# Kernel optimization log

Hardware: AMD Instinct MI355X
Metric: run time of the kernel (lower is better)

## Reference

```python
import jax, jax.numpy as jnp
import numpy as np

B, N, NH = 16, 2048, 64
DROP = 0.1


def setup_inputs() -> dict:
    key = jax.random.key(0)
    ks = jax.random.split(key, 10)
    s = 1.0 / np.sqrt(NH)
    return {
        "adj": jax.random.normal(ks[0], (B, N, N), jnp.float32) * 0.02,
        "diff": jax.random.normal(ks[1], (B, N, N), jnp.float32) * 0.02,
        "sub_local_pos1": jax.random.normal(ks[2], (B, N, NH), jnp.float32),
        "sub_local_pos2": jax.random.normal(ks[3], (B, N, NH), jnp.float32),
        "sub_local_neg1": jax.random.normal(ks[4], (B, N, NH), jnp.float32),
        "sub_local_neg2": jax.random.normal(ks[5], (B, N, NH), jnp.float32),
        # Bilinear params: weight [1, NH, NH], bias [1] (xavier-ish scale)
        "W0": jax.random.normal(ks[6], (1, NH, NH), jnp.float32) * s,
        "b0": jnp.zeros((1,), jnp.float32),
        "W1": jax.random.normal(ks[7], (1, NH, NH), jnp.float32) * s,
        "b1": jnp.zeros((1,), jnp.float32),
        "W2": jax.random.normal(ks[8], (1, NH, NH), jnp.float32) * s,
        "b2": jnp.zeros((1,), jnp.float32),
        "alpha": jnp.full((1,), 0.5, jnp.float32),
        "beta": jnp.full((1,), 0.5, jnp.float32),
        "lamda": jnp.full((1,), 0.5, jnp.float32),
        "k": 0.5,  # static fraction kept per topk cascade
    }


def _bilinear(x, y, W, b):
    # nn.Bilinear(NH, NH, 1): out[b,n] = x[b,n,:] @ W[0] @ y[b,n,:] + b[0]
    return jnp.einsum('bni,ij,bnj->bn', x, W[0], y) + b[0]


def _select(X, idx):
    # Select module: sort indices along batch dim 0, then per-row gather
    idx = jnp.sort(idx, axis=0)
    return jnp.take_along_axis(X, idx[:, :, None], axis=1)


def _topk_idx(logits, k_frac):
    half = logits.shape[1] // 2
    score = jax.nn.sigmoid(logits[:, half:] - logits[:, :half])  # neg - pos
    _, idx_pos = jax.lax.top_k(score, half)
    return idx_pos[:, : int(k_frac * half)]


def _forward(adj, diff, pos1, pos2, neg1, neg2,
             W0, b0, W1, b1, W2, b2, alpha, beta, lamda, k):
    mkey = jax.random.key(1)
    m1 = jax.random.uniform(jax.random.fold_in(mkey, 0), (N, NH)) < DROP
    m2 = jax.random.uniform(jax.random.fold_in(mkey, 1), (N, NH)) < DROP
    p1 = jnp.where(m1, 0.0, pos1); n1 = jnp.where(m1, 0.0, neg1)
    p2 = jnp.where(m2, 0.0, pos2); n2 = jnp.where(m2, 0.0, neg2)

    fus_pos = (p1 + p2) * 0.5
    fus_neg = (n1 + n2) * 0.5

    # Readout = mean over node dim, then sigmoid, broadcast back to [B,N,NH]
    g1 = jnp.broadcast_to(jax.nn.sigmoid(jnp.mean(p1, axis=1))[:, None, :], p1.shape)
    g2 = jnp.broadcast_to(jax.nn.sigmoid(jnp.mean(p2, axis=1))[:, None, :], p2.shape)

    lf1 = jnp.concatenate([_bilinear(fus_pos, g1, W0, b0), _bilinear(fus_neg, g1, W0, b0)], 1)
    lf2 = jnp.concatenate([_bilinear(fus_pos, g2, W0, b0), _bilinear(fus_neg, g2, W0, b0)], 1)
    logits_fusion = alpha * lf1 + (1.0 - alpha) * lf2  # [B, 2N]

    idx = _topk_idx(logits_fusion, k)  # [B, K1]

    sel_pos = _select(fus_pos, idx)
    sel_neg = _select(fus_neg, idx)
    l1 = _select(jax.nn.sigmoid(jnp.einsum('bnm,bmh->bnh', adj, p1)), idx)
    l2 = _select(jax.nn.sigmoid(jnp.einsum('bnm,bmh->bnh', diff, p2)), idx)

    ls1 = jnp.concatenate([_bilinear(sel_pos, l1, W1, b1), _bilinear(sel_neg, l1, W1, b1)], 1)
    ls2 = jnp.concatenate([_bilinear(sel_pos, l2, W1, b1), _bilinear(sel_neg, l2, W1, b1)], 1)
    logits_fusion_sub = beta * ls1 + (1.0 - beta) * ls2  # [B, 2*K1]

    idx_sub = _topk_idx(logits_fusion_sub, k)  # [B, K2]

    sel_pos_sub = _select(sel_pos, idx_sub)
    sel_neg_sub = _select(sel_neg, idx_sub)
    l1s = _select(_select(jax.nn.sigmoid(p1), idx), idx_sub)
    l2s = _select(_select(jax.nn.sigmoid(p2), idx), idx_sub)

    lss1 = jnp.concatenate([_bilinear(sel_pos_sub, l1s, W2, b2), _bilinear(sel_neg_sub, l1s, W2, b2)], 1)
    lss2 = jnp.concatenate([_bilinear(sel_pos_sub, l2s, W2, b2), _bilinear(sel_neg_sub, l2s, W2, b2)], 1)
    logits_fusion_sub_sub = lamda * lss1 + (1.0 - lamda) * lss2  # [B, 2*K2]

    return (logits_fusion, logits_fusion_sub, logits_fusion_sub_sub)


def reference(adj, diff, sub_local_pos1, sub_local_pos2, sub_local_neg1, sub_local_neg2,
              W0, b0, W1, b1, W2, b2, alpha, beta, lamda, k):
    return _forward(adj, diff, sub_local_pos1, sub_local_pos2, sub_local_neg1, sub_local_neg2,
                    W0, b0, W1, b1, W2, b2, alpha, beta, lamda, k)
```

## Files before the change

### kernel.cpp

```cpp
#include <hip/hip_runtime.h>
#include <cstdint>
#include <cstddef>

static constexpr int Bn  = 16;
static constexpr int Nn  = 2048;
static constexpr int NHn = 64;
static constexpr int K1  = 1024;
static constexpr int K2  = 512;

__host__ __device__ inline void tf2x32(uint32_t k0, uint32_t k1, uint32_t& x0, uint32_t& x1) {
  const uint32_t ks0 = k0, ks1 = k1, ks2 = k0 ^ k1 ^ 0x1BD11BDAu;
  x0 += ks0; x1 += ks1;
  const int R[20] = {13,15,26,6, 17,29,16,24, 13,15,26,6, 17,29,16,24, 13,15,26,6};
  const uint32_t ks[3] = {ks0, ks1, ks2};
  int inj = 0;
  for (int r = 0; r < 20; ++r) {
    x0 += x1;
    x1 = (x1 << R[r]) | (x1 >> (32 - R[r]));
    x1 ^= x0;
    if ((r & 3) == 3) {
      ++inj;
      x0 += ks[inj % 3];
      x1 += ks[(inj + 1) % 3] + (uint32_t)inj;
    }
  }
}

__device__ __forceinline__ float xla_expf(float x) {
  const float LOG2EF   = 1.44269504088896341f;
  const float ln2_hi   = 0.693359375f;
  const float nln2_lo  = 2.12194440e-4f;
  const float p0 = 1.9875691500e-4f, p1c = 1.3981999507e-3f, p2c = 8.3334519073e-3f,
              p3c = 4.1665795894e-2f, p4c = 1.6666665459e-1f, p5c = 5.0000001201e-1f;
  float xc = fminf(fmaxf(x, -87.33654785f), 88.72283935f);
  float m = floorf(__fmaf_rn(xc, LOG2EF, 0.5f));
  float r = __fmaf_rn(m, -ln2_hi, xc);
  r = __fmaf_rn(m, nln2_lo, r);
  float r2 = __fmul_rn(r, r);
  float y = p0;
  y = __fmaf_rn(y, r, p1c);
  y = __fmaf_rn(y, r, p2c);
  y = __fmaf_rn(y, r, p3c);
  y = __fmaf_rn(y, r, p4c);
  y = __fmaf_rn(y, r, p5c);
  y = __fmaf_rn(y, r2, r);
  y = __fadd_rn(y, 1.0f);
  int n = (int)m;
  float s2 = __uint_as_float((uint32_t)(n + 127) << 23);
  return __fmul_rn(y, s2);
}

__device__ __forceinline__ float sigmoid_exp(float x) {
  float e = xla_expf(-x);
  return __fdiv_rn(1.0f, __fadd_rn(1.0f, e));
}

__device__ __forceinline__ unsigned long long pack_key(float s, int idx) {
  return ((unsigned long long)(__float_as_uint(s) ^ 0xFFFFFFFFu) << 32) | (uint32_t)idx;
}

__global__ void mask_kernel(uint32_t fk0a, uint32_t fk1a, uint32_t fk0b, uint32_t fk1b,
                            float* __restrict__ mask1, float* __restrict__ mask2) {
  int i = blockIdx.x * blockDim.x + threadIdx.x;
  if (i >= Nn * NHn) return;
  uint32_t x0 = 0u, x1 = (uint32_t)i;
  tf2x32(fk0a, fk1a, x0, x1);
  uint32_t bits = x0 ^ x1;
  float u = __uint_as_float((bits >> 9) | 0x3f800000u) - 1.0f;
  mask1[i] = (u < 0.1f) ? 1.0f : 0.0f;
  x0 = 0u; x1 = (uint32_t)i;
  tf2x32(fk0b, fk1b, x0, x1);
  bits = x0 ^ x1;
  u = __uint_as_float((bits >> 9) | 0x3f800000u) - 1.0f;
  mask2[i] = (u < 0.1f) ? 1.0f : 0.0f;
}

__global__ void drop_kernel(const float* __restrict__ pos1, const float* __restrict__ pos2,
                            const float* __restrict__ mask1, const float* __restrict__ mask2,
                            float* __restrict__ p1, float* __restrict__ p2) {
  size_t i = (size_t)blockIdx.x * blockDim.x + threadIdx.x;
  int nh = (int)(i & (size_t)(Nn * NHn - 1));
  p1[i] = (mask1[nh] != 0.0f) ? 0.0f : pos1[i];
  p2[i] = (mask2[nh] != 0.0f) ? 0.0f : pos2[i];
}

__global__ void gmean_kernel(const float* __restrict__ p1, const float* __restrict__ p2,
                             float* __restrict__ g1, float* __restrict__ g2) {
  int b = blockIdx.x, h = threadIdx.x;
  const float* P1 = p1 + (size_t)b * Nn * NHn + h;
  const float* P2 = p2 + (size_t)b * Nn * NHn + h;
  float a1 = 0.0f, a2 = 0.0f;
  for (int n = 0; n < Nn; n += 8) {
    float v1[8], v2[8];
#pragma unroll
    for (int u = 0; u < 8; ++u) {
      v1[u] = P1[(size_t)(n + u) * NHn];
      v2[u] = P2[(size_t)(n + u) * NHn];
    }
#pragma unroll
    for (int u = 0; u < 8; ++u) {
      a1 = __fadd_rn(a1, v1[u]);
      a2 = __fadd_rn(a2, v2[u]);
    }
  }
  float m1 = __fdiv_rn(a1, 2048.0f);
  float m2 = __fdiv_rn(a2, 2048.0f);
  g1[b * 64 + h] = sigmoid_exp(m1);
  g2[b * 64 + h] = sigmoid_exp(m2);
}

__global__ __launch_bounds__(256) void logits1_np(
    const float* __restrict__ p1, const float* __restrict__ p2,
    const float* __restrict__ neg1, const float* __restrict__ neg2,
    const float* __restrict__ mask1, const float* __restrict__ mask2,
    const float* __restrict__ g1, const float* __restrict__ g2,
    const float* __restrict__ W0, const float* __restrict__ b0p,
    const float* __restrict__ alphap,
    float* __restrict__ out0, unsigned long long* __restrict__ key1) {
  __shared__ __align__(16) float xp[64][68], xn[64][68], w[4096], g[2][64];
  int b = blockIdx.y, n0 = blockIdx.x * 64, t = threadIdx.x;
  for (int c = 0; c < 16; ++c) {
    int idx = c * 256 + t, row = idx >> 6, i = idx & 63;
    size_t ga = ((size_t)b * Nn + n0 + row) * NHn + i;
    int ma = (n0 + row) * NHn + i;
    xp[row][i] = __fmul_rn(__fadd_rn(p1[ga], p2[ga]), 0.5f);
    float nv1 = (mask1[ma] != 0.0f) ? 0.0f : neg1[ga];
    float nv2 = (mask2[ma] != 0.0f) ? 0.0f : neg2[ga];
    xn[row][i] = __fmul_rn(__fadd_rn(nv1, nv2), 0.5f);
    w[idx] = W0[idx];
  }
  if (t < 64) { g[0][t] = g1[b * 64 + t]; g[1][t] = g2[b * 64 + t]; }
  __syncthreads();
  int row = t >> 2, e = t & 3;
  const float* x = (e & 2) ? &xn[row][0] : &xp[row][0];
  const float* gg = g[e & 1];
  float T[64];
#pragma unroll
  for (int j = 0; j < 64; ++j) T[j] = 0.0f;
  for (int i = 0; i < 64; ++i) {
    float xv = x[i];
#pragma unroll
    for (int jb = 0; jb < 16; ++jb) {
      float4 wv = *(const float4*)&w[i * 64 + jb * 4];
      T[jb * 4 + 0] = __fmaf_rn(xv, wv.x, T[jb * 4 + 0]);
      T[jb * 4 + 1] = __fmaf_rn(xv, wv.y, T[jb * 4 + 1]);
      T[jb * 4 + 2] = __fmaf_rn(xv, wv.z, T[jb * 4 + 2]);
      T[jb * 4 + 3] = __fmaf_rn(xv, wv.w, T[jb * 4 + 3]);
    }
  }
  float acc = 0.0f;
#pragma unroll
  for (int jb = 0; jb < 16; ++jb) {
    float4 gv = *(const float4*)&gg[jb * 4];
    acc = __fadd_rn(acc, __fmul_rn(T[jb * 4 + 0], gv.x));
    acc = __fadd_rn(acc, __fmul_rn(T[jb * 4 + 1], gv.y));
    acc = __fadd_rn(acc, __fmul_rn(T[jb * 4 + 2], gv.z));
    acc = __fadd_rn(acc, __fmul_rn(T[jb * 4 + 3], gv.w));
  }
  float a = __fadd_rn(acc, *b0p);
  float al = *alphap, om = __fsub_rn(1.0f, al);
  float other = __shfl_xor(a, 1);
  float L = __fadd_rn(__fmul_rn(al, a), __fmul_rn(om, other));
  float Lneg = __shfl_xor(L, 2);
  int n = n0 + row;
  if (e == 0) {
    out0[(size_t)b * (2 * Nn) + n] = L;
    float d = __fsub_rn(Lneg, L);
    key1[(size_t)b * Nn + n] = pack_key(sigmoid_exp(d), n);
  } else if (e == 2) {
    out0[(size_t)b * (2 * Nn) + Nn + n] = L;
  }
}

template <int S>
__global__ void topk_bitonic(const unsigned long long* __restrict__ keysrc,
                             int* __restrict__ idx_out) {
  constexpr int K = S / 2;
  __shared__ unsigned long long keys[S];
  int b = blockIdx.x;
  for (int i = threadIdx.x; i < S; i += blockDim.x)
    keys[i] = keysrc[(size_t)b * S + i];
  for (int k = 2; k <= S; k <<= 1) {
    for (int j = k >> 1; j > 0; j >>= 1) {
      __syncthreads();
      for (int t = threadIdx.x; t < S / 2; t += blockDim.x) {
        int i = ((t / j) * (j << 1)) + (t % j);
        unsigned long long a = keys[i], c = keys[i + j];
        if (((i & k) == 0) == (a > c)) { keys[i] = c; keys[i + j] = a; }
      }
    }
  }
  __syncthreads();
  for (int t = threadIdx.x; t < K; t += blockDim.x)
    idx_out[(size_t)b * K + t] = (int)(keys[t] & 0xffffffffu);
}

__global__ void colsort_kernel(const int* __restrict__ idx, int* __restrict__ sidx, int K) {
  int j = blockIdx.x * blockDim.x + threadIdx.x;
  if (j >= K) return;
  int v[16];
  for (int b = 0; b < 16; ++b) v[b] = idx[b * K + j];
  for (int a = 1; a < 16; ++a) {
    int x = v[a]; int c = a - 1;
    while (c >= 0 && v[c] > x) { v[c + 1] = v[c]; --c; }
    v[c + 1] = x;
  }
  for (int b = 0; b < 16; ++b) sidx[b * K + j] = v[b];
}

__global__ __launch_bounds__(256) void selmm_np3(const float* __restrict__ M,
                                                 const float* __restrict__ P,
                                                 const int* __restrict__ sidx,
                                                 float* __restrict__ L) {
  __shared__ __align__(16) float ash[32][132];
  __shared__ __align__(16) float psh[128][64];
  __shared__ int rj[32];
  int b = blockIdx.y, j0 = blockIdx.x * 32, t = threadIdx.x;
  if (t < 32) rj[t] = sidx[b * K1 + j0 + t];
  __syncthreads();
  int cg = t & 15, rg = t >> 4;
  int r0 = rg * 2, r1 = r0 + 1;
  const float* Mb = M + (size_t)b * Nn * Nn;
  const float* Pb = P + (size_t)b * Nn * NHn;
  float acc00 = 0.f, acc01 = 0.f, acc02 = 0.f, acc03 = 0.f;
  float acc10 = 0.f, acc11 = 0.f, acc12 = 0.f, acc13 = 0.f;
  for (int m0 = 0; m0 < Nn; m0 += 128) {
#pragma unroll
    for (int pass = 0; pass < 16; ++pass) {
      int idx = pass * 256 + t;
      int row = idx >> 7, col = idx & 127;
      ash[row][col] = Mb[(size_t)rj[row] * Nn + m0 + col];
    }
#pragma unroll 8
    for (int pass = 0; pass < 32; ++pass) {
      int idx = pass * 256 + t;
      int mm = idx >> 6, hh = idx & 63;
      psh[mm][hh] = Pb[(size_t)(m0 + mm) * NHn + hh];
    }
    __syncthreads();
#pragma unroll 4
    for (int mb = 0; mb < 32; ++mb) {
      float4 a0 = *(const float4*)&ash[r0][mb * 4];
      float4 a1 = *(const float4*)&ash[r1][mb * 4];
      float4 pv0 = *(const float4*)&psh[mb * 4 + 0][cg * 4];
      float4 pv1 = *(const float4*)&psh[mb * 4 + 1][cg * 4];
      float4 pv2 = *(const float4*)&psh[mb * 4 + 2][cg * 4];
      float4 pv3 = *(const float4*)&psh[mb * 4 + 3][cg * 4];
      acc00 = __fmaf_rn(a0.x, pv0.x, acc00);
      acc01 = __fmaf_rn(a0.x, pv0.y, acc01);
      acc02 = __fmaf_rn(a0.x, pv0.z, acc02);
      acc03 = __fmaf_rn(a0.x, pv0.w, acc03);
      acc10 = __fmaf_rn(a1.x, pv0.x, acc10);
      acc11 = __fmaf_rn(a1.x, pv0.y, acc11);
      acc12 = __fmaf_rn(a1.x, pv0.z, acc12);
      acc13 = __fmaf_rn(a1.x, pv0.w, acc13);
      acc00 = __fmaf_rn(a0.y, pv1.x, acc00);
      acc01 = __fmaf_rn(a0.y, pv1.y, acc01);
      acc02 = __fmaf_rn(a0.y, pv1.z, acc02);
      acc03 = __fmaf_rn(a0.y, pv1.w, acc03);
      acc10 = __fmaf_rn(a1.y, pv1.x, acc10);
      acc11 = __fmaf_rn(a1.y, pv1.y, acc11);
      acc12 = __fmaf_rn(a1.y, pv1.z, acc12);
      acc13 = __fmaf_rn(a1.y, pv1.w, acc13);
      acc00 = __fmaf_rn(a0.z, pv2.x, acc00);
      acc01 = __fmaf_rn(a0.z, pv2.y, acc01);
      acc02 = __fmaf_rn(a0.z, pv2.z, acc02);
      acc03 = __fmaf_rn(a0.z, pv2.w, acc03);
      acc10 = __fmaf_rn(a1.z, pv2.x, acc10);
      acc11 = __fmaf_rn(a1.z, pv2.y, acc11);
      acc12 = __fmaf_rn(a1.z, pv2.z, acc12);
      acc13 = __fmaf_rn(a1.z, pv2.w, acc13);
      acc00 = __fmaf_rn(a0.w, pv3.x, acc00);
      acc01 = __fmaf_rn(a0.w, pv3.y, acc01);
      acc02 = __fmaf_rn(a0.w, pv3.z, acc02);
      acc03 = __fmaf_rn(a0.w, pv3.w, acc03);
      acc10 = __fmaf_rn(a1.w, pv3.x, acc10);
      acc11 = __fmaf_rn(a1.w, pv3.y, acc11);
      acc12 = __fmaf_rn(a1.w, pv3.z, acc12);
      acc13 = __fmaf_rn(a1.w, pv3.w, acc13);
    }
    __syncthreads();
  }
  size_t base0 = ((size_t)b * K1 + j0 + r0) * NHn + cg * 4;
  size_t base1 = ((size_t)b * K1 + j0 + r1) * NHn + cg * 4;
  L[base0 + 0] = sigmoid_exp(acc00);
  L[base0 + 1] = sigmoid_exp(acc01);
  L[base0 + 2] = sigmoid_exp(acc02);
  L[base0 + 3] = sigmoid_exp(acc03);
  L[base1 + 0] = sigmoid_exp(acc10);
  L[base1 + 1] = sigmoid_exp(acc11);
  L[base1 + 2] = sigmoid_exp(acc12);
  L[base1 + 3] = sigmoid_exp(acc13);
}

__global__ __launch_bounds__(256) void logits2_np(
    const float* __restrict__ p1, const float* __restrict__ p2,
    const float* __restrict__ neg1, const float* __restrict__ neg2,
    const float* __restrict__ mask1, const float* __restrict__ mask2,
    const int* __restrict__ sidx1,
    const float* __restrict__ l1, const float* __restrict__ l2,
    const float* __restrict__ W1, const float* __restrict__ b1p,
    const float* __restrict__ betap,
    float* __restrict__ out1, unsigned long long* __restrict__ key2) {
  __shared__ __align__(16) float xp[64][68], xn[64][68], y1s[64][68], y2s[64][68], w[4096];
  __shared__ int rrs[64];
  int b = blockIdx.y, j0 = blockIdx.x * 64, t = threadIdx.x;
  if (t < 64) rrs[t] = sidx1[b * K1 + j0 + t];
  __syncthreads();
  for (int c = 0; c < 16; ++c) {
    int idx = c * 256 + t, row = idx >> 6, i = idx & 63;
    int rr = rrs[row];
    size_t ga = ((size_t)b * Nn + rr) * NHn + i;
    int ma = rr * NHn + i;
    xp[row][i] = __fmul_rn(__fadd_rn(p1[ga], p2[ga]), 0.5f);
    float nv1 = (mask1[ma] != 0.0f) ? 0.0f : neg1[ga];
    float nv2 = (mask2[ma] != 0.0f) ? 0.0f : neg2[ga];
    xn[row][i] = __fmul_rn(__fadd_rn(nv1, nv2), 0.5f);
    size_t la = ((size_t)b * K1 + j0 + row) * NHn + i;
    y1s[row][i] = l1[la];
    y2s[row][i] = l2[la];
    w[idx] = W1[idx];
  }
  __syncthreads();
  int row = t >> 2, e = t & 3;
  const float* x = (e & 2) ? &xn[row][0] : &xp[row][0];
  const float* yy = (e & 1) ? &y2s[row][0] : &y1s[row][0];
  float T[64];
#pragma unroll
  for (int j = 0; j < 64; ++j) T[j] = 0.0f;
  for (int i = 0; i < 64; ++i) {
    float xv = x[i];
#pragma unroll
    for (int jb = 0; jb < 16; ++jb) {
      float4 wv = *(const float4*)&w[i * 64 + jb * 4];
      T[jb * 4 + 0] = __fmaf_rn(xv, wv.x, T[jb * 4 + 0]);
      T[jb * 4 + 1] = __fmaf_rn(xv, wv.y, T[jb * 4 + 1]);
      T[jb * 4 + 2] = __fmaf_rn(xv, wv.z, T[jb * 4 + 2]);
      T[jb * 4 + 3] = __fmaf_rn(xv, wv.w, T[jb * 4 + 3]);
    }
  }
  float acc = 0.0f;
#pragma unroll
  for (int jb = 0; jb < 16; ++jb) {
    float4 yv = *(const float4*)&yy[jb * 4];
    acc = __fadd_rn(acc, __fmul_rn(T[jb * 4 + 0], yv.x));
    acc = __fadd_rn(acc, __fmul_rn(T[jb * 4 + 1], yv.y));
    acc = __fadd_rn(acc, __fmul_rn(T[jb * 4 + 2], yv.z));
    acc = __fadd_rn(acc, __fmul_rn(T[jb * 4 + 3], yv.w));
  }
  float a = __fadd_rn(acc, *b1p);
  float be = *betap, om = __fsub_rn(1.0f, be);
  float other = __shfl_xor(a, 1);
  float L = __fadd_rn(__fmul_rn(be, a), __fmul_rn(om, other));
  float Lneg = __shfl_xor(L, 2);
  int j = j0 + row;
  if (e == 0) {
    out1[(size_t)b * (2 * K1) + j] = L;
    float d = __fsub_rn(Lneg, L);
    key2[(size_t)b * K1 + j] = pack_key(sigmoid_exp(d), j);
  } else if (e == 2) {
    out1[(size_t)b * (2 * K1) + K1 + j] = L;
  }
}

__global__ void logits3_kernel(const float* __restrict__ p1, const float* __restrict__ p2,
                               const float* __restrict__ neg1, const float* __restrict__ neg2,
                               const float* __restrict__ mask1, const float* __restrict__ mask2,
                               const int* __restrict__ sidx1, const int* __restrict__ sidx2,
                               const float* __restrict__ W2,
                               const float* __restrict__ b2p, const float* __restrict__ lamp,
                               float* __restrict__ out2) {
  int b = blockIdx.y, tt = blockIdx.x, h = threadIdx.x;
  int rr = sidx1[b * K1 + sidx2[b * K2 + tt]];
  __shared__ float XP[64], XN[64];
  size_t xb = ((size_t)b * Nn + rr) * NHn + h;
  int ma = rr * NHn + h;
  float pv1 = p1[xb], pv2 = p2[xb];
  float nv1 = (mask1[ma] != 0.0f) ? 0.0f : neg1[xb];
  float nv2 = (mask2[ma] != 0.0f) ? 0.0f : neg2[xb];
  XP[h] = (pv1 + pv2) * 0.5f;
  XN[h] = (nv1 + nv2) * 0.5f;
  __syncthreads();
  float tp = 0.f, tn = 0.f;
#pragma unroll 8
  for (int i = 0; i < 64; ++i) {
    float ww = W2[i * 64 + h];
    tp = fmaf(XP[i], ww, tp);
    tn = fmaf(XN[i], ww, tn);
  }
  float y1 = sigmoid_exp(pv1);
  float y2 = sigmoid_exp(pv2);
  float p11 = tp * y1, p12 = tp * y2, p21 = tn * y1, p22 = tn * y2;
  for (int o = 32; o > 0; o >>= 1) {
    p11 += __shfl_down(p11, o);
    p12 += __shfl_down(p12, o);
    p21 += __shfl_down(p21, o);
    p22 += __shfl_down(p22, o);
  }
  if (h == 0) {
    float bb = *b2p, lm = *lamp;
    out2[(size_t)b * (2 * K2) + tt]      = lm * (p11 + bb) + (1.0f - lm) * (p12 + bb);
    out2[(size_t)b * (2 * K2) + K2 + tt] = lm * (p21 + bb) + (1.0f - lm) * (p22 + bb);
  }
}

extern "C" void kernel_launch(void* const* d_in, const int* in_sizes, int n_in,
                              void* d_out, int out_size, void* d_ws, size_t ws_size,
                              hipStream_t stream) {
  (void)in_sizes; (void)n_in; (void)out_size; (void)ws_size;

  const float* adj   = (const float*)d_in[0];
  const float* diff  = (const float*)d_in[1];
  const float* pos1  = (const float*)d_in[2];
  const float* pos2  = (const float*)d_in[3];
  const float* neg1  = (const float*)d_in[4];
  const float* neg2  = (const float*)d_in[5];
  const float* W0    = (const float*)d_in[6];
  const float* b0    = (const float*)d_in[7];
  const float* W1    = (const float*)d_in[8];
  const float* b1    = (const float*)d_in[9];
  const float* W2    = (const float*)d_in[10];
  const float* b2    = (const float*)d_in[11];
  const float* alpha = (const float*)d_in[12];
  const float* beta  = (const float*)d_in[13];
  const float* lamda = (const float*)d_in[14];

  float* out0 = (float*)d_out;
  float* out1 = out0 + Bn * 2 * Nn;
  float* out2 = out1 + Bn * 2 * K1;

  char* w = (char*)d_ws;
  size_t off = 0;
  auto alloc = [&](size_t bytes) -> void* {
    void* p = w + off;
    off += (bytes + 255) & ~(size_t)255;
    return p;
  };
  float* mask1 = (float*)alloc((size_t)Nn * NHn * 4);
  float* mask2 = (float*)alloc((size_t)Nn * NHn * 4);
  float* p1    = (float*)alloc((size_t)Bn * Nn * NHn * 4);
  float* p2    = (float*)alloc((size_t)Bn * Nn * NHn * 4);
  float* g1    = (float*)alloc((size_t)Bn * 64 * 4);
  float* g2    = (float*)alloc((size_t)Bn * 64 * 4);
  unsigned long long* key1 = (unsigned long long*)alloc((size_t)Bn * Nn * 8);
  unsigned long long* key2 = (unsigned long long*)alloc((size_t)Bn * K1 * 8);
  int*   idx1  = (int*)alloc((size_t)Bn * K1 * 4);
  int*   sidx1 = (int*)alloc((size_t)Bn * K1 * 4);
  int*   idx2  = (int*)alloc((size_t)Bn * K2 * 4);
  int*   sidx2 = (int*)alloc((size_t)Bn * K2 * 4);
  float* l1    = (float*)alloc((size_t)Bn * K1 * NHn * 4);
  float* l2    = (float*)alloc((size_t)Bn * K1 * NHn * 4);

  uint32_t fk0a = 0u, fk1a = 0u;
  { uint32_t x0 = 0u, x1 = 0u; tf2x32(0u, 1u, x0, x1); fk0a = x0; fk1a = x1; }
  uint32_t fk0b = 0u, fk1b = 0u;
  { uint32_t x0 = 0u, x1 = 1u; tf2x32(0u, 1u, x0, x1); fk0b = x0; fk1b = x1; }

  mask_kernel<<<(Nn * NHn + 255) / 256, 256, 0, stream>>>(fk0a, fk1a, fk0b, fk1b, mask1, mask2);

  drop_kernel<<<(Bn * Nn * NHn) / 256, 256, 0, stream>>>(pos1, pos2, mask1, mask2, p1, p2);

  gmean_kernel<<<Bn, 64, 0, stream>>>(p1, p2, g1, g2);

  logits1_np<<<dim3(Nn / 64, Bn), 256, 0, stream>>>(p1, p2, neg1, neg2, mask1, mask2,
                                                    g1, g2, W0, b0, alpha, out0, key1);

  topk_bitonic<2048><<<Bn, 1024, 0, stream>>>(key1, idx1);
  colsort_kernel<<<K1 / 256, 256, 0, stream>>>(idx1, sidx1, K1);

  selmm_np3<<<dim3(K1 / 32, Bn), 256, 0, stream>>>(adj, p1, sidx1, l1);
  selmm_np3<<<dim3(K1 / 32, Bn), 256, 0, stream>>>(diff, p2, sidx1, l2);

  logits2_np<<<dim3(K1 / 64, Bn), 256, 0, stream>>>(p1, p2, neg1, neg2, mask1, mask2,
                                                    sidx1, l1, l2, W1, b1, beta, out1, key2);

  topk_bitonic<1024><<<Bn, 512, 0, stream>>>(key2, idx2);
  colsort_kernel<<<K2 / 256, 256, 0, stream>>>(idx2, sidx2, K2);

  logits3_kernel<<<dim3(K2, Bn), 64, 0, stream>>>(p1, p2, neg1, neg2, mask1, mask2,
                                                  sidx1, sidx2, W2, b2, lamda, out2);
}
```

Before: 366.3 us.

## Vectorize loads, enlarge selmm tiles, and rework bilinear logits thread mapping

drop_kernel now moves data as float4, and gmean stages rows through shared memory with coalesced float4 loads instead of strided per-column reads. selmm now computes 64 rows per block with a 4x4 register tile and float4 global-to-shared copies, halving block count and increasing reuse of each P tile. logits1 and logits2 use 128 rows per block, and each thread computes both bilinear terms from one shared T vector. W and g/l vectors are read directly from global/L1 instead of being staged in shared memory. The changes add register pressure and move more traffic onto cache reads of W.

Measured after the change: 398.1 us. +8.7%, slower.

```diff
diff --git a/kernel.cpp b/kernel.cpp
--- a/kernel.cpp
+++ b/kernel.cpp
@@ -75,41 +75,58 @@
   mask2[i] = (u < 0.1f) ? 1.0f : 0.0f;
 }
 
-__global__ void drop_kernel(const float* __restrict__ pos1, const float* __restrict__ pos2,
-                            const float* __restrict__ mask1, const float* __restrict__ mask2,
-                            float* __restrict__ p1, float* __restrict__ p2) {
-  size_t i = (size_t)blockIdx.x * blockDim.x + threadIdx.x;
-  int nh = (int)(i & (size_t)(Nn * NHn - 1));
-  p1[i] = (mask1[nh] != 0.0f) ? 0.0f : pos1[i];
-  p2[i] = (mask2[nh] != 0.0f) ? 0.0f : pos2[i];
-}
-
-__global__ void gmean_kernel(const float* __restrict__ p1, const float* __restrict__ p2,
-                             float* __restrict__ g1, float* __restrict__ g2) {
-  int b = blockIdx.x, h = threadIdx.x;
-  const float* P1 = p1 + (size_t)b * Nn * NHn + h;
-  const float* P2 = p2 + (size_t)b * Nn * NHn + h;
+__global__ void drop_kernel(const float4* __restrict__ pos1, const float4* __restrict__ pos2,
+                            const float4* __restrict__ mask1, const float4* __restrict__ mask2,
+                            float4* __restrict__ p1, float4* __restrict__ p2) {
+  size_t i4 = (size_t)blockIdx.x * blockDim.x + threadIdx.x;
+  int nh4 = (int)(i4 & (size_t)(Nn * NHn / 4 - 1));
+  float4 m1 = mask1[nh4], m2 = mask2[nh4];
+  float4 a = pos1[i4], c = pos2[i4];
+  float4 o1, o2;
+  o1.x = (m1.x != 0.0f) ? 0.0f : a.x;  o1.y = (m1.y != 0.0f) ? 0.0f : a.y;
+  o1.z = (m1.z != 0.0f) ? 0.0f : a.z;  o1.w = (m1.w != 0.0f) ? 0.0f : a.w;
+  o2.x = (m2.x != 0.0f) ? 0.0f : c.x;  o2.y = (m2.y != 0.0f) ? 0.0f : c.y;
+  o2.z = (m2.z != 0.0f) ? 0.0f : c.z;  o2.w = (m2.w != 0.0f) ? 0.0f : c.w;
+  p1[i4] = o1;
+  p2[i4] = o2;
+}
+
+__global__ __launch_bounds__(256) void gmean_kernel(const float* __restrict__ p1,
+                                                    const float* __restrict__ p2,
+                                                    float* __restrict__ g1,
+                                                    float* __restrict__ g2) {
+  __shared__ __align__(16) float s1[32][64], s2[32][64];
+  int b = blockIdx.x, t = threadIdx.x;
+  const float* P1 = p1 + (size_t)b * Nn * NHn;
+  const float* P2 = p2 + (size_t)b * Nn * NHn;
   float a1 = 0.0f, a2 = 0.0f;
-  for (int n = 0; n < Nn; n += 8) {
-    float v1[8], v2[8];
-#pragma unroll
-    for (int u = 0; u < 8; ++u) {
-      v1[u] = P1[(size_t)(n + u) * NHn];
-      v2[u] = P2[(size_t)(n + u) * NHn];
-    }
-#pragma unroll
-    for (int u = 0; u < 8; ++u) {
-      a1 = __fadd_rn(a1, v1[u]);
-      a2 = __fadd_rn(a2, v2[u]);
-    }
-  }
-  float m1 = __fdiv_rn(a1, 2048.0f);
-  float m2 = __fdiv_rn(a2, 2048.0f);
-  g1[b * 64 + h] = sigmoid_exp(m1);
-  g2[b * 64 + h] = sigmoid_exp(m2);
-}
-
-__global__ __launch_bounds__(256) void logits1_np(
+  for (int c = 0; c < Nn / 32; ++c) {
+    __syncthreads();
+#pragma unroll
+    for (int ppp = 0; ppp < 2; ++ppp) {
+      int f = ppp * 256 + t;
+      int row = f >> 4, c4 = f & 15;
+      *(float4*)&s1[row][c4 * 4] = *(const float4*)&P1[(size_t)(c * 32 + row) * NHn + c4 * 4];
+      *(float4*)&s2[row][c4 * 4] = *(const float4*)&P2[(size_t)(c * 32 + row) * NHn + c4 * 4];
+    }
+    __syncthreads();
+    if (t < 64) {
+#pragma unroll
+      for (int u = 0; u < 32; ++u) {
+        a1 = __fadd_rn(a1, s1[u][t]);
+        a2 = __fadd_rn(a2, s2[u][t]);
+      }
+    }
+  }
+  if (t < 64) {
+    float m1 = __fdiv_rn(a1, 2048.0f);
+    float m2 = __fdiv_rn(a2, 2048.0f);
+    g1[b * 64 + t] = sigmoid_exp(m1);
+    g2[b * 64 + t] = sigmoid_exp(m2);
+  }
+}
+
+__global__ __launch_bounds__(256, 2) void logits1_np(
     const float* __restrict__ p1, const float* __restrict__ p2,
     const float* __restrict__ neg1, const float* __restrict__ neg2,
     const float* __restrict__ mask1, const float* __restrict__ mask2,
@@ -117,9 +134,9 @@
     const float* __restrict__ W0, const float* __restrict__ b0p,
     const float* __restrict__ alphap,
     float* __restrict__ out0, unsigned long long* __restrict__ key1) {
-  __shared__ __align__(16) float xp[64][68], xn[64][68], w[4096], g[2][64];
-  int b = blockIdx.y, n0 = blockIdx.x * 64, t = threadIdx.x;
-  for (int c = 0; c < 16; ++c) {
+  __shared__ __align__(16) float xp[128][68], xn[128][68];
+  int b = blockIdx.y, n0 = blockIdx.x * 128, t = threadIdx.x;
+  for (int c = 0; c < 32; ++c) {
     int idx = c * 256 + t, row = idx >> 6, i = idx & 63;
     size_t ga = ((size_t)b * Nn + n0 + row) * NHn + i;
     int ma = (n0 + row) * NHn + i;
@@ -127,13 +144,10 @@
     float nv1 = (mask1[ma] != 0.0f) ? 0.0f : neg1[ga];
     float nv2 = (mask2[ma] != 0.0f) ? 0.0f : neg2[ga];
     xn[row][i] = __fmul_rn(__fadd_rn(nv1, nv2), 0.5f);
-    w[idx] = W0[idx];
-  }
-  if (t < 64) { g[0][t] = g1[b * 64 + t]; g[1][t] = g2[b * 64 + t]; }
-  __syncthreads();
-  int row = t >> 2, e = t & 3;
-  const float* x = (e & 2) ? &xn[row][0] : &xp[row][0];
-  const float* gg = g[e & 1];
+  }
+  __syncthreads();
+  int row = t >> 1, e = t & 1;
+  const float* x = e ? &xn[row][0] : &xp[row][0];
   float T[64];
 #pragma unroll
   for (int j = 0; j < 64; ++j) T[j] = 0.0f;
@@ -141,33 +155,39 @@
     float xv = x[i];
 #pragma unroll
     for (int jb = 0; jb < 16; ++jb) {
-      float4 wv = *(const float4*)&w[i * 64 + jb * 4];
+      float4 wv = *(const float4*)&W0[i * 64 + jb * 4];
       T[jb * 4 + 0] = __fmaf_rn(xv, wv.x, T[jb * 4 + 0]);
       T[jb * 4 + 1] = __fmaf_rn(xv, wv.y, T[jb * 4 + 1]);
       T[jb * 4 + 2] = __fmaf_rn(xv, wv.z, T[jb * 4 + 2]);
       T[jb * 4 + 3] = __fmaf_rn(xv, wv.w, T[jb * 4 + 3]);
     }
   }
-  float acc = 0.0f;
+  const float* G1 = g1 + b * 64;
+  const float* G2 = g2 + b * 64;
+  float acc1 = 0.0f, acc2 = 0.0f;
 #pragma unroll
   for (int jb = 0; jb < 16; ++jb) {
-    float4 gv = *(const float4*)&gg[jb * 4];
-    acc = __fadd_rn(acc, __fmul_rn(T[jb * 4 + 0], gv.x));
-    acc = __fadd_rn(acc, __fmul_rn(T[jb * 4 + 1], gv.y));
-    acc = __fadd_rn(acc, __fmul_rn(T[jb * 4 + 2], gv.z));
-    acc = __fadd_rn(acc, __fmul_rn(T[jb * 4 + 3], gv.w));
-  }
-  float a = __fadd_rn(acc, *b0p);
-  float al = *alphap, om = __fsub_rn(1.0f, al);
-  float other = __shfl_xor(a, 1);
-  float L = __fadd_rn(__fmul_rn(al, a), __fmul_rn(om, other));
-  float Lneg = __shfl_xor(L, 2);
+    float4 gv1 = *(const float4*)&G1[jb * 4];
+    float4 gv2 = *(const float4*)&G2[jb * 4];
+    acc1 = __fadd_rn(acc1, __fmul_rn(T[jb * 4 + 0], gv1.x));
+    acc1 = __fadd_rn(acc1, __fmul_rn(T[jb * 4 + 1], gv1.y));
+    acc1 = __fadd_rn(acc1, __fmul_rn(T[jb * 4 + 2], gv1.z));
+    acc1 = __fadd_rn(acc1, __fmul_rn(T[jb * 4 + 3], gv1.w));
+    acc2 = __fadd_rn(acc2, __fmul_rn(T[jb * 4 + 0], gv2.x));
+    acc2 = __fadd_rn(acc2, __fmul_rn(T[jb * 4 + 1], gv2.y));
+    acc2 = __fadd_rn(acc2, __fmul_rn(T[jb * 4 + 2], gv2.z));
+    acc2 = __fadd_rn(acc2, __fmul_rn(T[jb * 4 + 3], gv2.w));
+  }
+  float b0 = *b0p, al = *alphap, om = __fsub_rn(1.0f, al);
+  float L = __fadd_rn(__fmul_rn(al, __fadd_rn(acc1, b0)),
+                      __fmul_rn(om, __fadd_rn(acc2, b0)));
+  float Lother = __shfl_xor(L, 1);
   int n = n0 + row;
   if (e == 0) {
     out0[(size_t)b * (2 * Nn) + n] = L;
-    float d = __fsub_rn(Lneg, L);
+    float d = __fsub_rn(Lother, L);
     key1[(size_t)b * Nn + n] = pack_key(sigmoid_exp(d), n);
-  } else if (e == 2) {
+  } else {
     out0[(size_t)b * (2 * Nn) + Nn + n] = L;
   }
 }
@@ -208,92 +228,85 @@
   for (int b = 0; b < 16; ++b) sidx[b * K + j] = v[b];
 }
 
-__global__ __launch_bounds__(256) void selmm_np3(const float* __restrict__ M,
+__global__ __launch_bounds__(256) void selmm_np4(const float* __restrict__ M,
                                                  const float* __restrict__ P,
                                                  const int* __restrict__ sidx,
                                                  float* __restrict__ L) {
-  __shared__ __align__(16) float ash[32][132];
+  __shared__ __align__(16) float ash[64][132];
   __shared__ __align__(16) float psh[128][64];
-  __shared__ int rj[32];
-  int b = blockIdx.y, j0 = blockIdx.x * 32, t = threadIdx.x;
-  if (t < 32) rj[t] = sidx[b * K1 + j0 + t];
+  __shared__ int rj[64];
+  int b = blockIdx.y, j0 = blockIdx.x * 64, t = threadIdx.x;
+  if (t < 64) rj[t] = sidx[b * K1 + j0 + t];
   __syncthreads();
   int cg = t & 15, rg = t >> 4;
-  int r0 = rg * 2, r1 = r0 + 1;
   const float* Mb = M + (size_t)b * Nn * Nn;
   const float* Pb = P + (size_t)b * Nn * NHn;
-  float acc00 = 0.f, acc01 = 0.f, acc02 = 0.f, acc03 = 0.f;
-  float acc10 = 0.f, acc11 = 0.f, acc12 = 0.f, acc13 = 0.f;
+  float acc[4][4];
+#pragma unroll
+  for (int r = 0; r < 4; ++r)
+#pragma unroll
+    for (int c = 0; c < 4; ++c) acc[r][c] = 0.0f;
+
   for (int m0 = 0; m0 < Nn; m0 += 128) {
 #pragma unroll
-    for (int pass = 0; pass < 16; ++pass) {
-      int idx = pass * 256 + t;
-      int row = idx >> 7, col = idx & 127;
-      ash[row][col] = Mb[(size_t)rj[row] * Nn + m0 + col];
-    }
-#pragma unroll 8
-    for (int pass = 0; pass < 32; ++pass) {
-      int idx = pass * 256 + t;
-      int mm = idx >> 6, hh = idx & 63;
-      psh[mm][hh] = Pb[(size_t)(m0 + mm) * NHn + hh];
+    for (int pass = 0; pass < 8; ++pass) {
+      int f = pass * 256 + t;
+      int row = f >> 5, c4 = f & 31;
+      *(float4*)&ash[row][c4 * 4] = *(const float4*)&Mb[(size_t)rj[row] * Nn + m0 + c4 * 4];
+    }
+#pragma unroll
+    for (int pass = 0; pass < 8; ++pass) {
+      int f = pass * 256 + t;
+      int mm = f >> 4, c4 = f & 15;
+      *(float4*)&psh[mm][c4 * 4] = *(const float4*)&Pb[(size_t)(m0 + mm) * NHn + c4 * 4];
     }
     __syncthreads();
 #pragma unroll 4
     for (int mb = 0; mb < 32; ++mb) {
-      float4 a0 = *(const float4*)&ash[r0][mb * 4];
-      float4 a1 = *(const float4*)&ash[r1][mb * 4];
+      float4 a0 = *(const float4*)&ash[rg * 4 + 0][mb * 4];
+      float4 a1 = *(const float4*)&ash[rg * 4 + 1][mb * 4];
+      float4 a2 = *(const float4*)&ash[rg * 4 + 2][mb * 4];
+      float4 a3 = *(const float4*)&ash[rg * 4 + 3][mb * 4];
       float4 pv0 = *(const float4*)&psh[mb * 4 + 0][cg * 4];
       float4 pv1 = *(const float4*)&psh[mb * 4 + 1][cg * 4];
       float4 pv2 = *(const float4*)&psh[mb * 4 + 2][cg * 4];
       float4 pv3 = *(const float4*)&psh[mb * 4 + 3][cg * 4];
-      acc00 = __fmaf_rn(a0.x, pv0.x, acc00);
-      acc01 = __fmaf_rn(a0.x, pv0.y, acc01);
-      acc02 = __fmaf_rn(a0.x, pv0.z, acc02);
-      acc03 = __fmaf_rn(a0.x, pv0.w, acc03);
-      acc10 = __fmaf_rn(a1.x, pv0.x, acc10);
-      acc11 = __fmaf_rn(a1.x, pv0.y, acc11);
-      acc12 = __fmaf_rn(a1.x, pv0.z, acc12);
-      acc13 = __fmaf_rn(a1.x, pv0.w, acc13);
-      acc00 = __fmaf_rn(a0.y, pv1.x, acc00);
-      acc01 = __fmaf_rn(a0.y, pv1.y, acc01);
-      acc02 = __fmaf_rn(a0.y, pv1.z, acc02);
-      acc03 = __fmaf_rn(a0.y, pv1.w, acc03);
-      acc10 = __fmaf_rn(a1.y, pv1.x, acc10);
-      acc11 = __fmaf_rn(a1.y, pv1.y, acc11);
-      acc12 = __fmaf_rn(a1.y, pv1.z, acc12);
-      acc13 = __fmaf_rn(a1.y, pv1.w, acc13);
-      acc00 = __fmaf_rn(a0.z, pv2.x, acc00);
-      acc01 = __fmaf_rn(a0.z, pv2.y, acc01);
-      acc02 = __fmaf_rn(a0.z, pv2.z, acc02);
-      acc03 = __fmaf_rn(a0.z, pv2.w, acc03);
-      acc10 = __fmaf_rn(a1.z, pv2.x, acc10);
-      acc11 = __fmaf_rn(a1.z, pv2.y, acc11);
-      acc12 = __fmaf_rn(a1.z, pv2.z, acc12);
-      acc13 = __fmaf_rn(a1.z, pv2.w, acc13);
-      acc00 = __fmaf_rn(a0.w, pv3.x, acc00);
-      acc01 = __fmaf_rn(a0.w, pv3.y, acc01);
-      acc02 = __fmaf_rn(a0.w, pv3.z, acc02);
-      acc03 = __fmaf_rn(a0.w, pv3.w, acc03);
-      acc10 = __fmaf_rn(a1.w, pv3.x, acc10);
-      acc11 = __fmaf_rn(a1.w, pv3.y, acc11);
-      acc12 = __fmaf_rn(a1.w, pv3.z, acc12);
-      acc13 = __fmaf_rn(a1.w, pv3.w, acc13);
+#define STEP(q, aq, pq)                                        \
+      acc[0][0] = __fmaf_rn(a0.aq, pq.x, acc[0][0]);           \
+      acc[0][1] = __fmaf_rn(a0.aq, pq.y, acc[0][1]);           \
+      acc[0][2] = __fmaf_rn(a0.aq, pq.z, acc[0][2]);           \
+      acc[0][3] = __fmaf_rn(a0.aq, pq.w, acc[0][3]);           \
+      acc[1][0] = __fmaf_rn(a1.aq, pq.x, acc[1][0]);           \
+      acc[1][1] = __fmaf_rn(a1.aq, pq.y, acc[1][1]);           \
+      acc[1][2] = __fmaf_rn(a1.aq, pq.z, acc[1][2]);           \
+      acc[1][3] = __fmaf_rn(a1.aq, pq.w, acc[1][3]);           \
+      acc[2][0] = __fmaf_rn(a2.aq, pq.x, acc[2][0]);           \
+      acc[2][1] = __fmaf_rn(a2.aq, pq.y, acc[2][1]);           \
+      acc[2][2] = __fmaf_rn(a2.aq, pq.z, acc[2][2]);           \
+      acc[2][3] = __fmaf_rn(a2.aq, pq.w, acc[2][3]);           \
+      acc[3][0] = __fmaf_rn(a3.aq, pq.x, acc[3][0]);           \
+      acc[3][1] = __fmaf_rn(a3.aq, pq.y, acc[3][1]);           \
+      acc[3][2] = __fmaf_rn(a3.aq, pq.z, acc[3][2]);           \
+      acc[3][3] = __fmaf_rn(a3.aq, pq.w, acc[3][3]);
+      STEP(0, x, pv0)
+      STEP(1, y, pv1)
+      STEP(2, z, pv2)
+      STEP(3, w, pv3)
+#undef STEP
     }
     __syncthreads();
   }
-  size_t base0 = ((size_t)b * K1 + j0 + r0) * NHn + cg * 4;
-  size_t base1 = ((size_t)b * K1 + j0 + r1) * NHn + cg * 4;
-  L[base0 + 0] = sigmoid_exp(acc00);
-  L[base0 + 1] = sigmoid_exp(acc01);
-  L[base0 + 2] = sigmoid_exp(acc02);
-  L[base0 + 3] = sigmoid_exp(acc03);
-  L[base1 + 0] = sigmoid_exp(acc10);
-  L[base1 + 1] = sigmoid_exp(acc11);
-  L[base1 + 2] = sigmoid_exp(acc12);
-  L[base1 + 3] = sigmoid_exp(acc13);
-}
-
-__global__ __launch_bounds__(256) void logits2_np(
+#pragma unroll
+  for (int r = 0; r < 4; ++r) {
+    size_t base = ((size_t)b * K1 + j0 + rg * 4 + r) * NHn + cg * 4;
+    L[base + 0] = sigmoid_exp(acc[r][0]);
+    L[base + 1] = sigmoid_exp(acc[r][1]);
+    L[base + 2] = sigmoid_exp(acc[r][2]);
+    L[base + 3] = sigmoid_exp(acc[r][3]);
+  }
+}
+
+__global__ __launch_bounds__(256, 2) void logits2_np(
     const float* __restrict__ p1, const float* __restrict__ p2,
     const float* __restrict__ neg1, const float* __restrict__ neg2,
     const float* __restrict__ mask1, const float* __restrict__ mask2,
@@ -302,12 +315,12 @@
     const float* __restrict__ W1, const float* __restrict__ b1p,
     const float* __restrict__ betap,
     float* __restrict__ out1, unsigned long long* __restrict__ key2) {
-  __shared__ __align__(16) float xp[64][68], xn[64][68], y1s[64][68], y2s[64][68], w[4096];
-  __shared__ int rrs[64];
-  int b = blockIdx.y, j0 = blockIdx.x * 64, t = threadIdx.x;
-  if (t < 64) rrs[t] = sidx1[b * K1 + j0 + t];
-  __syncthreads();
-  for (int c = 0; c < 16; ++c) {
+  __shared__ __align__(16) float xp[128][68], xn[128][68];
+  __shared__ int rrs[128];
+  int b = blockIdx.y, j0 = blockIdx.x * 128, t = threadIdx.x;
+  if (t < 128) rrs[t] = sidx1[b * K1 + j0 + t];
+  __syncthreads();
+  for (int c = 0; c < 32; ++c) {
     int idx = c * 256 + t, row = idx >> 6, i = idx & 63;
     int rr = rrs[row];
     size_t ga = ((size_t)b * Nn + rr) * NHn + i;
@@ -316,15 +329,10 @@
     float nv1 = (mask1[ma] != 0.0f) ? 0.0f : neg1[ga];
     float nv2 = (mask2[ma] != 0.0f) ? 0.0f : neg2[ga];
     xn[row][i] = __fmul_rn(__fadd_rn(nv1, nv2), 0.5f);
-    size_t la = ((size_t)b * K1 + j0 + row) * NHn + i;
-    y1s[row][i] = l1[la];
-    y2s[row][i] = l2[la];
-    w[idx] = W1[idx];
-  }
-  __syncthreads();
-  int row = t >> 2, e = t & 3;
-  const float* x = (e & 2) ? &xn[row][0] : &xp[row][0];
-  const float* yy = (e & 1) ? &y2s[row][0] : &y1s[row][0];
+  }
+  __syncthreads();
+  int row = t >> 1, e = t & 1;
+  const float* x = e ? &xn[row][0] : &xp[row][0];
   float T[64];
 #pragma unroll
   for (int j = 0; j < 64; ++j) T[j] = 0.0f;
@@ -332,33 +340,39 @@
     float xv = x[i];
 #pragma unroll
     for (int jb = 0; jb < 16; ++jb) {
-      float4 wv = *(const float4*)&w[i * 64 + jb * 4];
+      float4 wv = *(const float4*)&W1[i * 64 + jb * 4];
       T[jb * 4 + 0] = __fmaf_rn(xv, wv.x, T[jb * 4 + 0]);
       T[jb * 4 + 1] = __fmaf_rn(xv, wv.y, T[jb * 4 + 1]);
       T[jb * 4 + 2] = __fmaf_rn(xv, wv.z, T[jb * 4 + 2]);
       T[jb * 4 + 3] = __fmaf_rn(xv, wv.w, T[jb * 4 + 3]);
     }
   }
-  float acc = 0.0f;
+  const float* Y1 = l1 + ((size_t)b * K1 + j0 + row) * NHn;
+  const float* Y2 = l2 + ((size_t)b * K1 + j0 + row) * NHn;
+  float acc1 = 0.0f, acc2 = 0.0f;
 #pragma unroll
   for (int jb = 0; jb < 16; ++jb) {
-    float4 yv = *(const float4*)&yy[jb * 4];
-    acc = __fadd_rn(acc, __fmul_rn(T[jb * 4 + 0], yv.x));
-    acc = __fadd_rn(acc, __fmul_rn(T[jb * 4 + 1], yv.y));
-    acc = __fadd_rn(acc, __fmul_rn(T[jb * 4 + 2], yv.z));
-    acc = __fadd_rn(acc, __fmul_rn(T[jb * 4 + 3], yv.w));
-  }
-  float a = __fadd_rn(acc, *b1p);
-  float be = *betap, om = __fsub_rn(1.0f, be);
-  float other = __shfl_xor(a, 1);
-  float L = __fadd_rn(__fmul_rn(be, a), __fmul_rn(om, other));
-  float Lneg = __shfl_xor(L, 2);
+    float4 yv1 = *(const float4*)&Y1[jb * 4];
+    float4 yv2 = *(const float4*)&Y2[jb * 4];
+    acc1 = __fadd_rn(acc1, __fmul_rn(T[jb * 4 + 0], yv1.x));
+    acc1 = __fadd_rn(acc1, __fmul_rn(T[jb * 4 + 1], yv1.y));
+    acc1 = __fadd_rn(acc1, __fmul_rn(T[jb * 4 + 2], yv1.z));
+    acc1 = __fadd_rn(acc1, __fmul_rn(T[jb * 4 + 3], yv1.w));
+    acc2 = __fadd_rn(acc2, __fmul_rn(T[jb * 4 + 0], yv2.x));
+    acc2 = __fadd_rn(acc2, __fmul_rn(T[jb * 4 + 1], yv2.y));
+    acc2 = __fadd_rn(acc2, __fmul_rn(T[jb * 4 + 2], yv2.z));
+    acc2 = __fadd_rn(acc2, __fmul_rn(T[jb * 4 + 3], yv2.w));
+  }
+  float bb = *b1p, be = *betap, om = __fsub_rn(1.0f, be);
+  float L = __fadd_rn(__fmul_rn(be, __fadd_rn(acc1, bb)),
+                      __fmul_rn(om, __fadd_rn(acc2, bb)));
+  float Lother = __shfl_xor(L, 1);
   int j = j0 + row;
   if (e == 0) {
     out1[(size_t)b * (2 * K1) + j] = L;
-    float d = __fsub_rn(Lneg, L);
+    float d = __fsub_rn(Lother, L);
     key2[(size_t)b * K1 + j] = pack_key(sigmoid_exp(d), j);
-  } else if (e == 2) {
+  } else {
     out1[(size_t)b * (2 * K1) + K1 + j] = L;
   }
 }
@@ -458,21 +472,23 @@
 
   mask_kernel<<<(Nn * NHn + 255) / 256, 256, 0, stream>>>(fk0a, fk1a, fk0b, fk1b, mask1, mask2);
 
-  drop_kernel<<<(Bn * Nn * NHn) / 256, 256, 0, stream>>>(pos1, pos2, mask1, mask2, p1, p2);
-
-  gmean_kernel<<<Bn, 64, 0, stream>>>(p1, p2, g1, g2);
-
-  logits1_np<<<dim3(Nn / 64, Bn), 256, 0, stream>>>(p1, p2, neg1, neg2, mask1, mask2,
-                                                    g1, g2, W0, b0, alpha, out0, key1);
+  drop_kernel<<<(Bn * Nn * NHn / 4) / 256, 256, 0, stream>>>(
+      (const float4*)pos1, (const float4*)pos2, (const float4*)mask1, (const float4*)mask2,
+      (float4*)p1, (float4*)p2);
+
+  gmean_kernel<<<Bn, 256, 0, stream>>>(p1, p2, g1, g2);
+
+  logits1_np<<<dim3(Nn / 128, Bn), 256, 0, stream>>>(p1, p2, neg1, neg2, mask1, mask2,
+                                                     g1, g2, W0, b0, alpha, out0, key1);
 
   topk_bitonic<2048><<<Bn, 1024, 0, stream>>>(key1, idx1);
   colsort_kernel<<<K1 / 256, 256, 0, stream>>>(idx1, sidx1, K1);
 
-  selmm_np3<<<dim3(K1 / 32, Bn), 256, 0, stream>>>(adj, p1, sidx1, l1);
-  selmm_np3<<<dim3(K1 / 32, Bn), 256, 0, stream>>>(diff, p2, sidx1, l2);
-
-  logits2_np<<<dim3(K1 / 64, Bn), 256, 0, stream>>>(p1, p2, neg1, neg2, mask1, mask2,
-                                                    sidx1, l1, l2, W1, b1, beta, out1, key2);
+  selmm_np4<<<dim3(K1 / 64, Bn), 256, 0, stream>>>(adj, p1, sidx1, l1);
+  selmm_np4<<<dim3(K1 / 64, Bn), 256, 0, stream>>>(diff, p2, sidx1, l2);
+
+  logits2_np<<<dim3(K1 / 128, Bn), 256, 0, stream>>>(p1, p2, neg1, neg2, mask1, mask2,
+                                                     sidx1, l1, l2, W1, b1, beta, out1, key2);
 
   topk_bitonic<1024><<<Bn, 512, 0, stream>>>(key2, idx2);
   colsort_kernel<<<K2 / 256, 256, 0, stream>>>(idx2, sidx2, K2);
```
